# Kernel optimization log

Hardware: AMD Instinct MI355X
Metric: run time of the kernel (lower is better)

Reference implementation:

```python
import jax, jax.numpy as jnp
import numpy as np
import math

B, N, D = 128, 64, 2
H, M, L = 64, 64, 2
OMEGA = 1.0


def setup_inputs() -> dict:
    key = jax.random.key(0)
    ks = jax.random.split(key, 32)
    s = 0.1  # param scale
    rn = lambda k, shp: jax.random.normal(k, shp, dtype=jnp.float32) * s
    inp = {
        "x": jax.random.normal(ks[0], (B, N, D), dtype=jnp.float32),
        "spin": jnp.zeros((B, N, 1), jnp.float32),
        "node_w1": rn(ks[1], (D + 1, H)), "node_b1": rn(ks[2], (H,)),
        "node_w2": rn(ks[3], (H, H)), "node_b2": rn(ks[4], (H,)),
        "edge_w1": rn(ks[5], (D + 2, M)), "edge_b1": rn(ks[6], (M,)),
        "edge_w2": rn(ks[7], (M, M)), "edge_b2": rn(ks[8], (M,)),
        "v2e_w1": rn(ks[9], (L, H + M, M)), "v2e_b1": rn(ks[10], (L, M)),
        "v2e_w2": rn(ks[11], (L, M, M)), "v2e_b2": rn(ks[12], (L, M)),
        "e2v_w1": rn(ks[13], (L, M, H)), "e2v_b1": rn(ks[14], (L, H)),
        "e2v_w2": rn(ks[15], (L, H, H)), "e2v_b2": rn(ks[16], (L, H)),
        "head_w1": rn(ks[17], (H, H)), "head_b1": rn(ks[18], (H,)),
        "head_w2": rn(ks[19], (H, D)), "head_b2": rn(ks[20], (D,)),
        # bf_scale_init=0.3 -> softplus-inverse
        "scale": jnp.array([math.log(math.exp(0.3) - 1.0)], jnp.float32),
    }
    return inp


def _mlp(x, w1, b1, w2, b2, act):
    return act(x @ w1 + b1) @ w2 + b2


def reference(x, spin, node_w1, node_b1, node_w2, node_b2,
              edge_w1, edge_b1, edge_w2, edge_b2,
              v2e_w1, v2e_b1, v2e_w2, v2e_b2,
              e2v_w1, e2v_b1, e2v_w2, e2v_b2,
              head_w1, head_b1, head_w2, head_b2, scale):
    gelu = lambda t: jax.nn.gelu(t, approximate=False)  # torch exact GELU
    b, n, d = x.shape
    xs = x * jnp.float32(math.sqrt(OMEGA))
    # node embedding: [B,N,H]
    hv = _mlp(jnp.concatenate([xs, spin], -1), node_w1, node_b1, node_w2, node_b2, gelu)
    # dense pairwise edge features; dr[b,i,j] = xs[b,j] - xs[b,i]
    dr = xs[:, None, :, :] - xs[:, :, None, :]            # [B,N,N,D]
    r2 = jnp.sum(dr * dr, axis=-1, keepdims=True)          # [B,N,N,1]
    rr = jnp.sqrt(r2 + 1e-12)
    he = _mlp(jnp.concatenate([dr, rr, r2], -1), edge_w1, edge_b1, edge_w2, edge_b2, gelu)  # [B,N,N,M]
    # mask excludes self-edges (i==j) from aggregation (they were never created
    # in the original edge list; their dense entries never influence off-diag values)
    mask = (1.0 - jnp.eye(n, dtype=x.dtype))[None, :, :, None]
    inv = jnp.float32(1.0 / max(n - 1, 1))
    for l in range(v2e_w1.shape[0]):
        hvb = jnp.broadcast_to(hv[:, :, None, :], (b, n, n, hv.shape[-1]))  # source node i
        he = _mlp(jnp.concatenate([hvb, he], -1), v2e_w1[l], v2e_b1[l], v2e_w2[l], v2e_b2[l], gelu)
        m = _mlp(he, e2v_w1[l], e2v_b1[l], e2v_w2[l], e2v_b2[l], gelu)      # [B,N,N,H]
        hv = hv + jnp.sum(m * mask, axis=1) * inv           # scatter-add over sources i into j
    dx = _mlp(hv, head_w1, head_b1, head_w2, head_b2, jnp.tanh) * jax.nn.softplus(scale[0])
    return dx - jnp.mean(dx, axis=1, keepdims=True)
```

## Files before the change

kernel.cpp:

```cpp
#include <hip/hip_runtime.h>
#include <math.h>


typedef unsigned short u16;
typedef unsigned int u32;
typedef _Float16 half8 __attribute__((ext_vector_type(8)));
typedef __attribute__((ext_vector_type(4))) float floatx4;

#define TS 72
#define HROW 72
#define HBLK (64 * HROW)

__device__ __forceinline__ float gelu_f(float x) {
    float u = x * 0.70710678118654752f;
    float s = fabsf(u);
    float t = __builtin_amdgcn_rcpf(fmaf(0.47047f, s, 1.0f));
    float P = t * fmaf(t, fmaf(t, 0.7478556f, -0.0958798f), 0.3480242f);
    float r = copysignf(fmaf(-P, __expf(-s * s), 1.0f), u);
    return 0.5f * x * (1.0f + r);
}

__global__ __launch_bounds__(256) void k_pre1(
    const float* __restrict__ ew2, const float* __restrict__ w1he0,
    const float* __restrict__ w2_0, const float* __restrict__ u1_0,
    const float* __restrict__ w1he1, const float* __restrict__ w2_1,
    const float* __restrict__ u1_1,
    const float* __restrict__ eb2, const float* __restrict__ b2_0,
    const float* __restrict__ c1_0, const float* __restrict__ b2_1,
    const float* __restrict__ c1_1,
    const float* __restrict__ b1_0v, const float* __restrict__ b1nv,
    const float* __restrict__ u2_0, const float* __restrict__ u2_1,
    const float* __restrict__ w1n, const float* __restrict__ hw1,
    _Float16* __restrict__ WF,
    float* __restrict__ biasA, float* __restrict__ biasB,
    float* __restrict__ biasC, float* __restrict__ biasD,
    float* __restrict__ u2_0T, float* __restrict__ u2_1T,
    float* __restrict__ w1nT, float* __restrict__ hw1T)
{
    int blk = blockIdx.x;
    if (blk < 64) {
        int s = blk >> 4;
        int idx = (blk & 15) * 256 + threadIdx.x;
        int k = idx >> 6, n = idx & 63;
        const float *A, *Bm;
        if (s == 0)      { A = ew2;  Bm = w1he0; }
        else if (s == 1) { A = w2_0; Bm = u1_0;  }
        else if (s == 2) { A = w2_0; Bm = w1he1; }
        else             { A = w2_1; Bm = u1_1;  }
        float acc = 0.f;
        for (int q = 0; q < 64; ++q) acc = fmaf(A[k * 64 + q], Bm[q * 64 + n], acc);
        int kc = k >> 5, qd = (k >> 3) & 3, jj = k & 7;
        WF[(((s * 2 + kc) * 64 + n) * 4 + qd) * 8 + jj] = (_Float16)acc;
    } else if (blk == 64) {
        int s = threadIdx.x >> 6, cc = threadIdx.x & 63;
        const float *bv, *Bm, *add; float* dst;
        if (s == 0)      { bv = eb2;  Bm = w1he0; add = b1_0v; dst = biasA; }
        else if (s == 1) { bv = b2_0; Bm = u1_0;  add = c1_0;  dst = biasB; }
        else if (s == 2) { bv = b2_0; Bm = w1he1; add = b1nv;  dst = biasC; }
        else             { bv = b2_1; Bm = u1_1;  add = c1_1;  dst = biasD; }
        float acc = add[cc];
        for (int q = 0; q < 64; ++q) acc = fmaf(bv[q], Bm[q * 64 + cc], acc);
        dst[cc] = acc;
    } else {
        int idx = (blk - 65) * 256 + threadIdx.x;
        int s = idx >> 12, r = idx & 4095, m = r >> 6, tc = r & 63;
        const float* W = s == 0 ? u2_0 : s == 1 ? u2_1 : s == 2 ? w1n : hw1;
        float* WT      = s == 0 ? u2_0T : s == 1 ? u2_1T : s == 2 ? w1nT : hw1T;
        WT[tc * 64 + m] = W[m * 64 + tc];
    }
}

__global__ __launch_bounds__(256) void k_pre2(
    const float* __restrict__ x, const float* __restrict__ spin,
    const float* __restrict__ nw1, const float* __restrict__ nb1,
    const float* __restrict__ nw2, const float* __restrict__ nb2,
    const float* __restrict__ w1_0,
    const float* __restrict__ biasA,
    float* __restrict__ hv, float* __restrict__ p0)
{
    __shared__ float a[4][64];
    __shared__ float shv[4][64];
    int w = threadIdx.x >> 6, h = threadIdx.x & 63;
    int node = blockIdx.x * 4 + w;
    float2 xv = ((const float2*)x)[node];
    float sp = spin[node];
    float z = fmaf(xv.x, nw1[h], fmaf(xv.y, nw1[64 + h], fmaf(sp, nw1[128 + h], nb1[h])));
    a[w][h] = gelu_f(z);
    float acc = nb2[h];
    for (int k = 0; k < 64; ++k) acc = fmaf(a[w][k], nw2[k * 64 + h], acc);
    hv[node * 64 + h] = acc;
    shv[w][h] = acc;
    float pa = biasA[h];
    for (int k = 0; k < 64; ++k) pa = fmaf(shv[w][k], w1_0[k * 64 + h], pa);
    p0[node * 64 + h] = pa;
}

__device__ __forceinline__ void mfma_acc(
    const _Float16* __restrict__ tA, const _Float16* __restrict__ WF,
    int stage, int c, int quad, int nn, floatx4 acc[4])
{
    int sA = ((nn >> 2) & 3) << 3;
    #pragma unroll
    for (int kc = 0; kc < 2; ++kc) {
        half8 bf = *(const half8*)(WF + (((stage * 2 + kc) * 64 + c) * 4 + quad) * 8);
        int k0 = (kc * 32 + quad * 8) ^ sA;
        #pragma unroll
        for (int mt = 0; mt < 4; ++mt) {
            half8 af = *(const half8*)(tA + (mt * 16 + nn) * TS + k0);
            acc[mt] = __builtin_amdgcn_mfma_f32_16x16x32_f16(af, bf, acc[mt], 0, 0, 0);
        }
    }
}

__device__ __forceinline__ void init_bias(floatx4 acc[4], float bc) {
    #pragma unroll
    for (int mt = 0; mt < 4; ++mt) acc[mt] = (floatx4){bc, bc, bc, bc};
}
__device__ __forceinline__ void init_p(floatx4 acc[4], const float* __restrict__ p,
                                       int rowbase, int c, int quad) {
    #pragma unroll
    for (int mt = 0; mt < 4; ++mt)
        #pragma unroll
        for (int r = 0; r < 4; ++r)
            acc[mt][r] = p[(rowbase + mt * 16 + quad * 4 + r) * 64 + c];
}

__global__ __launch_bounds__(256, 8) void k_L0(
    const float* __restrict__ x,
    const float* __restrict__ ew1, const float* __restrict__ eb1,
    const float* __restrict__ p0,
    const float* __restrict__ biasB,
    const float* __restrict__ u2_0T, const float* __restrict__ c2_0,
    const _Float16* __restrict__ WF,
    const float* __restrict__ hv0, float* __restrict__ hv1,
    const float* __restrict__ w1nT, const float* __restrict__ biasC,
    float* __restrict__ p1,
    u16* __restrict__ he0g)
{
    __shared__ __align__(16) _Float16 tA[64 * TS];
    __shared__ float sS[64];
    __shared__ float shv[64];
    __shared__ float sred[256];
    int t = threadIdx.x, L = t & 63;
    int w = __builtin_amdgcn_readfirstlane(t >> 6);
    int nn = L & 15, quad = L >> 4;
    int c = w * 16 + nn;
    int cw = c ^ (quad << 3);
    int b = blockIdx.x >> 6, j = blockIdx.x & 63;

    float2 xi = ((const float2*)x)[b * 64 + L];
    float2 xj = ((const float2*)x)[b * 64 + j];
    float d0 = xj.x - xi.x, d1 = xj.y - xi.y;
    float r2 = fmaf(d0, d0, d1 * d1);
    float rr = sqrtf(r2 + 1e-12f);
    int swL = ((L >> 2) & 3) << 3;

    #pragma unroll
    for (int mb = 0; mb < 2; ++mb) {
        int m0 = w * 16 + mb * 8;
        half8 h8;
        #pragma unroll
        for (int kk = 0; kk < 8; ++kk) {
            int m = m0 + kk;
            float z = fmaf(d0, ew1[m], fmaf(d1, ew1[64 + m],
                      fmaf(rr, ew1[128 + m], fmaf(r2, ew1[192 + m], eb1[m]))));
            h8[kk] = (_Float16)gelu_f(z);
        }
        *(half8*)(tA + L * TS + (m0 ^ swL)) = h8;
    }
    __syncthreads();

    floatx4 acc[4];
    init_p(acc, p0, b * 64, c, quad);
    mfma_acc(tA, WF, 0, c, quad, nn, acc);
    __syncthreads();
    {
        u16* dst = he0g + (size_t)blockIdx.x * HBLK;
        #pragma unroll
        for (int mt = 0; mt < 4; ++mt)
            #pragma unroll
            for (int r = 0; r < 4; ++r) {
                int i = mt * 16 + quad * 4 + r;
                _Float16 y = (_Float16)gelu_f(acc[mt][r]);
                tA[i * TS + cw] = y;
                dst[i * HROW + cw] = __builtin_bit_cast(u16, y);
            }
    }
    __syncthreads();
    init_bias(acc, biasB[c]);
    mfma_acc(tA, WF, 1, c, quad, nn, acc);
    {
        float s = 0.f;
        #pragma unroll
        for (int mt = 0; mt < 4; ++mt)
            #pragma unroll
            for (int r = 0; r < 4; ++r) {
                int i = mt * 16 + quad * 4 + r;
                float g = gelu_f(acc[mt][r]);
                s += (i == j) ? 0.f : g;
            }
        s += __shfl_xor(s, 16);
        s += __shfl_xor(s, 32);
        if (quad == 0) sS[c] = s;
    }
    __syncthreads();
    {
        const float4* sv4 = (const float4*)(sS + w * 16);
        const float4* uv4 = (const float4*)(u2_0T + L * 64 + w * 16);
        float g = 0.f;
        #pragma unroll
        for (int m4 = 0; m4 < 4; ++m4) {
            float4 sv = sv4[m4], uv = uv4[m4];
            g = fmaf(sv.x, uv.x, fmaf(sv.y, uv.y, fmaf(sv.z, uv.z, fmaf(sv.w, uv.w, g))));
        }
        sred[w * 64 + L] = g;
    }
    __syncthreads();
    if (t < 64) {
        float g = sred[t] + sred[64 + t] + sred[128 + t] + sred[192 + t];
        int o = blockIdx.x * 64 + t;
        float hvv = hv0[o] + g * (1.0f / 63.0f) + c2_0[t];
        hv1[o] = hvv;
        shv[t] = hvv;
    }
    __syncthreads();
    {
        const float4* hv4 = (const float4*)(shv + w * 16);
        const float4* wv4 = (const float4*)(w1nT + L * 64 + w * 16);
        float pa = 0.f;
        #pragma unroll
        for (int m4 = 0; m4 < 4; ++m4) {
            float4 sv = hv4[m4], uv = wv4[m4];
            pa = fmaf(sv.x, uv.x, fmaf(sv.y, uv.y, fmaf(sv.z, uv.z, fmaf(sv.w, uv.w, pa))));
        }
        sred[w * 64 + L] = pa;
    }
    __syncthreads();
    if (t < 64)
        p1[blockIdx.x * 64 + t] = biasC[t] + sred[t] + sred[64 + t] + sred[128 + t] + sred[192 + t];
}

__global__ __launch_bounds__(256, 8) void k_L1(
    const u16* __restrict__ he0g,
    const float* __restrict__ p1,
    const float* __restrict__ biasD,
    const float* __restrict__ u2_1T, const float* __restrict__ c2_1,
    const _Float16* __restrict__ WF,
    const float* __restrict__ hv1,
    const float* __restrict__ hw1T, const float* __restrict__ hb1,
    const float* __restrict__ hw2, const float* __restrict__ hb2,
    const float* __restrict__ scale, float* __restrict__ dx)
{
    __shared__ __align__(16) _Float16 tA[64 * TS];
    __shared__ float sS[64];
    __shared__ float shv[64];
    __shared__ float sred[256];
    int t = threadIdx.x, L = t & 63;
    int w = __builtin_amdgcn_readfirstlane(t >> 6);
    int nn = L & 15, quad = L >> 4;
    int c = w * 16 + nn;
    int cw = c ^ (quad << 3);
    int b = blockIdx.x >> 6, j = blockIdx.x & 63;

    {
        const float4* src = (const float4*)(he0g + (size_t)blockIdx.x * HBLK);
        float4* dstl = (float4*)tA;
        for (int q = t; q < (HBLK * 2 / 16); q += 256)
            dstl[q] = src[q];
    }
    __syncthreads();

    floatx4 acc[4];
    init_p(acc, p1, b * 64, c, quad);
    mfma_acc(tA, WF, 2, c, quad, nn, acc);
    __syncthreads();
    #pragma unroll
    for (int mt = 0; mt < 4; ++mt)
        #pragma unroll
        for (int r = 0; r < 4; ++r)
            tA[(mt * 16 + quad * 4 + r) * TS + cw] = (_Float16)gelu_f(acc[mt][r]);
    __syncthreads();
    init_bias(acc, biasD[c]);
    mfma_acc(tA, WF, 3, c, quad, nn, acc);
    {
        float s = 0.f;
        #pragma unroll
        for (int mt = 0; mt < 4; ++mt)
            #pragma unroll
            for (int r = 0; r < 4; ++r) {
                int i = mt * 16 + quad * 4 + r;
                float g = gelu_f(acc[mt][r]);
                s += (i == j) ? 0.f : g;
            }
        s += __shfl_xor(s, 16);
        s += __shfl_xor(s, 32);
        if (quad == 0) sS[c] = s;
    }
    __syncthreads();
    {
        const float4* sv4 = (const float4*)(sS + w * 16);
        const float4* uv4 = (const float4*)(u2_1T + L * 64 + w * 16);
        float g = 0.f;
        #pragma unroll
        for (int m4 = 0; m4 < 4; ++m4) {
            float4 sv = sv4[m4], uv = uv4[m4];
            g = fmaf(sv.x, uv.x, fmaf(sv.y, uv.y, fmaf(sv.z, uv.z, fmaf(sv.w, uv.w, g))));
        }
        sred[w * 64 + L] = g;
    }
    __syncthreads();
    if (t < 64) {
        float g = sred[t] + sred[64 + t] + sred[128 + t] + sred[192 + t];
        float hv2 = hv1[blockIdx.x * 64 + t] + g * (1.0f / 63.0f) + c2_1[t];
        shv[t] = hv2;
    }
    __syncthreads();
    {
        const float4* hv4 = (const float4*)(shv + w * 16);
        const float4* wv4 = (const float4*)(hw1T + L * 64 + w * 16);
        float a = 0.f;
        #pragma unroll
        for (int m4 = 0; m4 < 4; ++m4) {
            float4 sv = hv4[m4], uv = wv4[m4];
            a = fmaf(sv.x, uv.x, fmaf(sv.y, uv.y, fmaf(sv.z, uv.z, fmaf(sv.w, uv.w, a))));
        }
        sred[w * 64 + L] = a;
    }
    __syncthreads();
    if (t < 64) {
        float a = hb1[t] + sred[t] + sred[64 + t] + sred[128 + t] + sred[192 + t];
        sS[t] = tanhf(a);
    }
    __syncthreads();
    if (t < 64) {
        float t1 = sS[t];
        float dd0 = t1 * hw2[t * 2], dd1 = t1 * hw2[t * 2 + 1];
        #pragma unroll
        for (int off = 1; off <= 32; off <<= 1) { dd0 += __shfl_xor(dd0, off); dd1 += __shfl_xor(dd1, off); }
        if (t == 0) {
            float sp = log1pf(__expf(scale[0]));
            dx[blockIdx.x * 2 + 0] = (dd0 + hb2[0]) * sp;
            dx[blockIdx.x * 2 + 1] = (dd1 + hb2[1]) * sp;
        }
    }
}

__global__ __launch_bounds__(64) void k_mean(
    const float* __restrict__ dx, float* __restrict__ out)
{
    __shared__ float s0[64], s1[64];
    int b = blockIdx.x, j = threadIdx.x;
    float2 d = ((const float2*)dx)[b * 64 + j];
    s0[j] = d.x; s1[j] = d.y;
    __syncthreads();
    float m0 = 0.f, m1 = 0.f;
    for (int q = 0; q < 64; ++q) { m0 += s0[q]; m1 += s1[q]; }
    ((float2*)out)[b * 64 + j] = make_float2(d.x - m0 * (1.0f / 64.0f), d.y - m1 * (1.0f / 64.0f));
}

__global__ void k_beacon(float* out, float code) { out[0] = code; }

extern "C" void kernel_launch(void* const* d_in, const int* in_sizes, int n_in,
                              void* d_out, int out_size, void* d_ws, size_t ws_size,
                              hipStream_t stream)
{
    static const int exp_sizes[23] = {
        16384, 8192, 192, 64, 4096, 64,
        256, 64, 4096, 64,
        16384, 128, 8192, 128,
        8192, 128, 8192, 128,
        4096, 64, 128, 2, 1
    };
    float* hv0 = (float*)d_ws;
    float* hv1 = hv0 + 524288;
    float* p0  = hv1 + 524288;
    float* p1  = p0  + 524288;
    float* dx  = p1  + 524288;
    float* u2_0T = dx + 16384;
    float* u2_1T = u2_0T + 4096;
    float* w1nT  = u2_1T + 4096;
    float* hw1T  = w1nT + 4096;
    float* biasA = hw1T + 4096;
    float* biasB = biasA + 64;
    float* biasC = biasB + 64;
    float* biasD = biasC + 64;
    _Float16* WF = (_Float16*)(biasD + 64);
    u16* he0g  = (u16*)(WF + 16384);
    const size_t need = (size_t)((char*)(he0g + (size_t)8192 * HBLK) - (char*)d_ws);

    int bad = -1;
    if (n_in != 23 || out_size != 16384) bad = 98;
    else if (ws_size < need) bad = 97;
    else for (int i = 0; i < 23; ++i)
        if (in_sizes[i] != exp_sizes[i]) { bad = i; break; }
    if (bad >= 0) {
        k_beacon<<<1, 1, 0, stream>>>((float*)d_out, 2e6f + bad * 1e4f);
        return;
    }

    const float* x      = (const float*)d_in[0];
    const float* spin   = (const float*)d_in[1];
    const float* nw1    = (const float*)d_in[2];
    const float* nb1    = (const float*)d_in[3];
    const float* nw2    = (const float*)d_in[4];
    const float* nb2    = (const float*)d_in[5];
    const float* ew1    = (const float*)d_in[6];
    const float* eb1    = (const float*)d_in[7];
    const float* ew2    = (const float*)d_in[8];
    const float* eb2    = (const float*)d_in[9];
    const float* v2e_w1 = (const float*)d_in[10];
    const float* v2e_b1 = (const float*)d_in[11];
    const float* v2e_w2 = (const float*)d_in[12];
    const float* v2e_b2 = (const float*)d_in[13];
    const float* e2v_w1 = (const float*)d_in[14];
    const float* e2v_b1 = (const float*)d_in[15];
    const float* e2v_w2 = (const float*)d_in[16];
    const float* e2v_b2 = (const float*)d_in[17];
    const float* hw1    = (const float*)d_in[18];
    const float* hb1    = (const float*)d_in[19];
    const float* hw2    = (const float*)d_in[20];
    const float* hb2    = (const float*)d_in[21];
    const float* scale  = (const float*)d_in[22];

    k_pre1<<<129, 256, 0, stream>>>(
        ew2, v2e_w1 + 4096, v2e_w2, e2v_w1,
        v2e_w1 + 12288, v2e_w2 + 4096, e2v_w1 + 4096,
        eb2, v2e_b2, e2v_b1, v2e_b2 + 64, e2v_b1 + 64,
        v2e_b1, v2e_b1 + 64,
        e2v_w2, e2v_w2 + 4096, v2e_w1 + 8192, hw1,
        WF, biasA, biasB, biasC, biasD,
        u2_0T, u2_1T, w1nT, hw1T);
    k_pre2<<<2048, 256, 0, stream>>>(x, spin, nw1, nb1, nw2, nb2,
                                     v2e_w1, biasA, hv0, p0);
    k_L0<<<8192, 256, 0, stream>>>(x, ew1, eb1,
        p0, biasB, u2_0T, e2v_b2,
        WF, hv0, hv1,
        w1nT, biasC, p1,
        he0g);
    k_L1<<<8192, 256, 0, stream>>>(he0g,
        p1, biasD, u2_1T, e2v_b2 + 64,
        WF, hv1, hw1T, hb1, hw2, hb2, scale, dx);
    k_mean<<<128, 64, 0, stream>>>(dx, (float*)d_out);
}
```

Before: 227.3 us.

## Merge weight-prep and node-embedding kernels; use cheaper rational GELU approximation

Folds the node-embedding kernel into the weight-preprocessing kernel as extra blocks, removing one launch. Each node block now recomputes the biasA term itself, so the dependency on the earlier bias block goes away. The GELU erf approximation switches from the exp-based form to a quartic rational form that avoids the exp. This GELU is used in the hot edge kernels and may lose some accuracy, and the redundant 64x64 bias dot per node block adds work.

New measurement: 226.9 us. Within noise of the previous version (-0.2%).

```diff
diff --git a/kernel.cpp b/kernel.cpp
--- a/kernel.cpp
+++ b/kernel.cpp
@@ -12,15 +12,15 @@
 #define HBLK (64 * HROW)
 
 __device__ __forceinline__ float gelu_f(float x) {
-    float u = x * 0.70710678118654752f;
-    float s = fabsf(u);
-    float t = __builtin_amdgcn_rcpf(fmaf(0.47047f, s, 1.0f));
-    float P = t * fmaf(t, fmaf(t, 0.7478556f, -0.0958798f), 0.3480242f);
-    float r = copysignf(fmaf(-P, __expf(-s * s), 1.0f), u);
-    return 0.5f * x * (1.0f + r);
-}
-
-__global__ __launch_bounds__(256) void k_pre1(
+    float s = fabsf(x) * 0.70710678118654752f;
+    float q = fmaf(fmaf(fmaf(fmaf(0.078108f, s, 0.000972f), s, 0.230389f), s, 0.278393f), s, 1.0f);
+    float q2 = q * q;
+    float r = __builtin_amdgcn_rcpf(q2 * q2);
+    float t = 0.5f * x * r;
+    return x > 0.f ? x - t : t;
+}
+
+__global__ __launch_bounds__(256) void k_pre(
     const float* __restrict__ ew2, const float* __restrict__ w1he0,
     const float* __restrict__ w2_0, const float* __restrict__ u1_0,
     const float* __restrict__ w1he1, const float* __restrict__ w2_1,
@@ -32,10 +32,14 @@
     const float* __restrict__ u2_0, const float* __restrict__ u2_1,
     const float* __restrict__ w1n, const float* __restrict__ hw1,
     _Float16* __restrict__ WF,
-    float* __restrict__ biasA, float* __restrict__ biasB,
-    float* __restrict__ biasC, float* __restrict__ biasD,
+    float* __restrict__ biasB, float* __restrict__ biasC, float* __restrict__ biasD,
     float* __restrict__ u2_0T, float* __restrict__ u2_1T,
-    float* __restrict__ w1nT, float* __restrict__ hw1T)
+    float* __restrict__ w1nT, float* __restrict__ hw1T,
+    const float* __restrict__ x, const float* __restrict__ spin,
+    const float* __restrict__ nw1, const float* __restrict__ nb1,
+    const float* __restrict__ nw2, const float* __restrict__ nb2,
+    const float* __restrict__ w1_0,
+    float* __restrict__ hv, float* __restrict__ p0)
 {
     int blk = blockIdx.x;
     if (blk < 64) {
@@ -53,46 +57,39 @@
         WF[(((s * 2 + kc) * 64 + n) * 4 + qd) * 8 + jj] = (_Float16)acc;
     } else if (blk == 64) {
         int s = threadIdx.x >> 6, cc = threadIdx.x & 63;
-        const float *bv, *Bm, *add; float* dst;
-        if (s == 0)      { bv = eb2;  Bm = w1he0; add = b1_0v; dst = biasA; }
-        else if (s == 1) { bv = b2_0; Bm = u1_0;  add = c1_0;  dst = biasB; }
-        else if (s == 2) { bv = b2_0; Bm = w1he1; add = b1nv;  dst = biasC; }
-        else             { bv = b2_1; Bm = u1_1;  add = c1_1;  dst = biasD; }
-        float acc = add[cc];
-        for (int q = 0; q < 64; ++q) acc = fmaf(bv[q], Bm[q * 64 + cc], acc);
-        dst[cc] = acc;
-    } else {
+        if (s > 0) {
+            const float *bv, *Bm, *add; float* dst;
+            if (s == 1)      { bv = b2_0; Bm = u1_0;  add = c1_0; dst = biasB; }
+            else if (s == 2) { bv = b2_0; Bm = w1he1; add = b1nv; dst = biasC; }
+            else             { bv = b2_1; Bm = u1_1;  add = c1_1; dst = biasD; }
+            float acc = add[cc];
+            for (int q = 0; q < 64; ++q) acc = fmaf(bv[q], Bm[q * 64 + cc], acc);
+            dst[cc] = acc;
+        }
+    } else if (blk < 129) {
         int idx = (blk - 65) * 256 + threadIdx.x;
         int s = idx >> 12, r = idx & 4095, m = r >> 6, tc = r & 63;
         const float* W = s == 0 ? u2_0 : s == 1 ? u2_1 : s == 2 ? w1n : hw1;
         float* WT      = s == 0 ? u2_0T : s == 1 ? u2_1T : s == 2 ? w1nT : hw1T;
         WT[tc * 64 + m] = W[m * 64 + tc];
-    }
-}
-
-__global__ __launch_bounds__(256) void k_pre2(
-    const float* __restrict__ x, const float* __restrict__ spin,
-    const float* __restrict__ nw1, const float* __restrict__ nb1,
-    const float* __restrict__ nw2, const float* __restrict__ nb2,
-    const float* __restrict__ w1_0,
-    const float* __restrict__ biasA,
-    float* __restrict__ hv, float* __restrict__ p0)
-{
-    __shared__ float a[4][64];
-    __shared__ float shv[4][64];
-    int w = threadIdx.x >> 6, h = threadIdx.x & 63;
-    int node = blockIdx.x * 4 + w;
-    float2 xv = ((const float2*)x)[node];
-    float sp = spin[node];
-    float z = fmaf(xv.x, nw1[h], fmaf(xv.y, nw1[64 + h], fmaf(sp, nw1[128 + h], nb1[h])));
-    a[w][h] = gelu_f(z);
-    float acc = nb2[h];
-    for (int k = 0; k < 64; ++k) acc = fmaf(a[w][k], nw2[k * 64 + h], acc);
-    hv[node * 64 + h] = acc;
-    shv[w][h] = acc;
-    float pa = biasA[h];
-    for (int k = 0; k < 64; ++k) pa = fmaf(shv[w][k], w1_0[k * 64 + h], pa);
-    p0[node * 64 + h] = pa;
+    } else {
+        __shared__ float a[4][64];
+        __shared__ float shv[4][64];
+        int w = threadIdx.x >> 6, h = threadIdx.x & 63;
+        int node = (blk - 129) * 4 + w;
+        float2 xv = ((const float2*)x)[node];
+        float sp = spin[node];
+        float z = fmaf(xv.x, nw1[h], fmaf(xv.y, nw1[64 + h], fmaf(sp, nw1[128 + h], nb1[h])));
+        a[w][h] = gelu_f(z);
+        float acc = nb2[h];
+        for (int k = 0; k < 64; ++k) acc = fmaf(a[w][k], nw2[k * 64 + h], acc);
+        hv[node * 64 + h] = acc;
+        shv[w][h] = acc;
+        float pa = b1_0v[h];
+        for (int q = 0; q < 64; ++q) pa = fmaf(eb2[q], w1he0[q * 64 + h], pa);
+        for (int k = 0; k < 64; ++k) pa = fmaf(shv[w][k], w1_0[k * 64 + h], pa);
+        p0[node * 64 + h] = pa;
+    }
 }
 
 __device__ __forceinline__ void mfma_acc(
@@ -380,8 +377,7 @@
     float* u2_1T = u2_0T + 4096;
     float* w1nT  = u2_1T + 4096;
     float* hw1T  = w1nT + 4096;
-    float* biasA = hw1T + 4096;
-    float* biasB = biasA + 64;
+    float* biasB = hw1T + 4096;
     float* biasC = biasB + 64;
     float* biasD = biasC + 64;
     _Float16* WF = (_Float16*)(biasD + 64);
@@ -422,16 +418,15 @@
     const float* hb2    = (const float*)d_in[21];
     const float* scale  = (const float*)d_in[22];
 
-    k_pre1<<<129, 256, 0, stream>>>(
+    k_pre<<<2177, 256, 0, stream>>>(
         ew2, v2e_w1 + 4096, v2e_w2, e2v_w1,
         v2e_w1 + 12288, v2e_w2 + 4096, e2v_w1 + 4096,
         eb2, v2e_b2, e2v_b1, v2e_b2 + 64, e2v_b1 + 64,
         v2e_b1, v2e_b1 + 64,
         e2v_w2, e2v_w2 + 4096, v2e_w1 + 8192, hw1,
-        WF, biasA, biasB, biasC, biasD,
-        u2_0T, u2_1T, w1nT, hw1T);
-    k_pre2<<<2048, 256, 0, stream>>>(x, spin, nw1, nb1, nw2, nb2,
-                                     v2e_w1, biasA, hv0, p0);
+        WF, biasB, biasC, biasD,
+        u2_0T, u2_1T, w1nT, hw1T,
+        x, spin, nw1, nb1, nw2, nb2, v2e_w1, hv0, p0);
     k_L0<<<8192, 256, 0, stream>>>(x, ew1, eb1,
         p0, biasB, u2_0T, e2v_b2,
         WF, hv0, hv1,
```
